# Performance work log

Hardware: AMD Instinct MI355X
Metric: run time of the kernel (lower is better)

The kernel has to match this reference:

```python
import jax, jax.numpy as jnp
import numpy as np

NUM_HEADS = 16


def setup_inputs() -> dict:
    key = jax.random.key(0)
    k1, k2, k3 = jax.random.split(key, 3)
    B, N, C = 2, 2048, 1024
    x = jax.random.normal(k1, (B, N, C), dtype=jnp.float32)
    w_qkv = jax.random.normal(k2, (3 * C, C), dtype=jnp.float32) * (C ** -0.5)
    w_proj = jax.random.normal(k3, (C, C), dtype=jnp.float32) * (C ** -0.5)
    b_proj = jnp.zeros((C,), dtype=jnp.float32)
    return {"x": x, "w_qkv": w_qkv, "w_proj": w_proj, "b_proj": b_proj}


def reference(x, w_qkv, w_proj, b_proj):
    B, N, C = x.shape
    H = NUM_HEADS
    D = C // H
    scale = 1.0 / jnp.sqrt(jnp.asarray(D, x.dtype))
    qkv = (x @ w_qkv.T).reshape(B, N, 3, H, D)
    qkv = jnp.transpose(qkv, (2, 0, 3, 1, 4))  # [3,B,H,N,D]
    q, k, v = qkv[0], qkv[1], qkv[2]
    # scaled dot-product attention with explicit score matrix [B,H,N,N]
    attn = jnp.einsum('bhnd,bhmd->bhnm', q, k) * scale
    attn = jax.nn.softmax(attn, axis=-1)
    out = jnp.einsum('bhnm,bhmd->bhnd', attn, v)
    out = jnp.transpose(out, (0, 2, 1, 3)).reshape(B, N, C)
    # output projection
    return out @ w_proj.T + b_proj
```

## Files before the change

kernel.cpp:

```cpp
#include <hip/hip_runtime.h>

typedef unsigned short u16;
typedef __attribute__((ext_vector_type(8))) short bf16x8;
typedef __attribute__((ext_vector_type(4))) float f32x4;

#define B_ 2
#define N_ 2048
#define C_ 1024
#define H_ 16
#define D_ 64
#define M_ (B_ * N_)

#define QSCALE 0.18033688011114336f

__device__ __forceinline__ u16 f2bf(float f) {
    union { float f; unsigned u; } x; x.f = f;
    return (u16)((x.u + 0x8000u) >> 16);
}
__device__ __forceinline__ unsigned pack2bf(float a, float b) {
    union { float f; unsigned u; } x, y; x.f = a; y.f = b;
    return __builtin_amdgcn_perm(y.u + 0x8000u, x.u + 0x8000u, 0x07060302);
}

__device__ __forceinline__ void async_copy16(const void* gsrc, void* ldst) {
    __builtin_amdgcn_global_load_lds(
        (__attribute__((address_space(1))) void*)gsrc,
        (__attribute__((address_space(3))) void*)ldst,
        16, 0, 0);
}

__global__ void cast3_kernel(const float* __restrict__ x, const float* __restrict__ wq,
                             const float* __restrict__ wp, u16* __restrict__ xo,
                             u16* __restrict__ wqo, u16* __restrict__ wpo) {
    int b = blockIdx.x;
    const float* s; u16* d;
    if (b < 4096)      { s = x;  d = xo;  }
    else if (b < 7168) { s = wq; d = wqo; b -= 4096; }
    else               { s = wp; d = wpo; b -= 7168; }
    int i = (b * 256 + threadIdx.x) * 4;
    const float4 v = *(const float4*)(s + i);
    uint2 o;
    o.x = pack2bf(v.x, v.y);
    o.y = pack2bf(v.z, v.w);
    *(uint2*)(d + i) = o;
}

template <int EPI>
__global__ __launch_bounds__(256, 2) void gemm_bt(
    const u16* __restrict__ A, const u16* __restrict__ Bm,
    int M, int Ncols, int K, int ntiles_n,
    u16* __restrict__ qo, u16* __restrict__ ko, u16* __restrict__ vo,
    const float* __restrict__ bias, float* __restrict__ out) {
    __shared__ u16 As[128 * 64];
    __shared__ u16 Bs[128 * 64];
    const int tid = threadIdx.x, lane = tid & 63, w = tid >> 6;
    const int bx = blockIdx.x % ntiles_n, by = blockIdx.x / ntiles_n;
    const int m0 = by * 128, n0 = bx * 128;
    const int wm = w >> 1, wn = w & 1;
    const int q16 = lane >> 4, l15 = lane & 15;
    const int r0 = lane >> 3, c0 = (lane & 7) * 8;
    f32x4 acc[4][4] = {};

    for (int k0 = 0; k0 < K; k0 += 64) {
#pragma unroll
        for (int i = 0; i < 4; ++i) {
            int blk = w * 4 + i;
            int r = blk * 8 + r0;
            async_copy16(A + (size_t)(m0 + r) * K + k0 + c0, (char*)As + blk * 1024);
            async_copy16(Bm + (size_t)(n0 + r) * K + k0 + c0, (char*)Bs + blk * 1024);
        }
        __builtin_amdgcn_s_waitcnt(0);
        __syncthreads();
#pragma unroll
        for (int ks = 0; ks < 2; ++ks) {
            bf16x8 af[4], bf[4];
#pragma unroll
            for (int i = 0; i < 4; ++i) {
                af[i] = *(const bf16x8*)&As[(wm * 64 + i * 16 + l15) * 64 + ks * 32 + q16 * 8];
                bf[i] = *(const bf16x8*)&Bs[(wn * 64 + i * 16 + l15) * 64 + ks * 32 + q16 * 8];
            }
#pragma unroll
            for (int mi = 0; mi < 4; ++mi)
#pragma unroll
                for (int ni = 0; ni < 4; ++ni)
                    acc[mi][ni] = __builtin_amdgcn_mfma_f32_16x16x32_bf16(af[mi], bf[ni], acc[mi][ni], 0, 0, 0);
        }
        __syncthreads();
    }

#pragma unroll
    for (int mi = 0; mi < 4; ++mi) {
#pragma unroll
        for (int ni = 0; ni < 4; ++ni) {
            int n_g = n0 + wn * 64 + ni * 16 + l15;
#pragma unroll
            for (int r = 0; r < 4; ++r) {
                int m_g = m0 + wm * 64 + mi * 16 + q16 * 4 + r;
                float v = acc[mi][ni][r];
                if (EPI == 0) {
                    int which = n_g >> 10;
                    int h = (n_g >> 6) & 15;
                    int d = n_g & 63;
                    int b = m_g >> 11;
                    int nn = m_g & 2047;
                    size_t idx = ((size_t)((b * H_ + h) * N_ + nn) << 6) + d;
                    if (which == 0)      qo[idx] = f2bf(v * QSCALE);
                    else if (which == 1) ko[idx] = f2bf(v);
                    else                 vo[idx] = f2bf(v);
                } else {
                    out[(size_t)m_g * Ncols + n_g] = v + bias[n_g];
                }
            }
        }
    }
}

__global__ __launch_bounds__(256) void transpose_v(const u16* __restrict__ V, u16* __restrict__ VT) {
    __shared__ u16 tile[64][72];
    const int t = threadIdx.x;
    const int bh = blockIdx.x >> 5;
    const int key0 = (blockIdx.x & 31) * 64;
    const size_t base = (size_t)bh * N_ * D_;
    const int r0 = t >> 3, c8 = (t & 7) * 8;
#pragma unroll
    for (int it = 0; it < 2; ++it) {
        int r = it * 32 + r0;
        uint4 d4 = *(const uint4*)(V + base + (size_t)(key0 + r) * D_ + c8);
        *(uint4*)&tile[r][c8] = d4;
    }
    __syncthreads();
#pragma unroll
    for (int it = 0; it < 2; ++it) {
        int d = it * 32 + r0;
        unsigned t0 = tile[c8 + 0][d], t1 = tile[c8 + 1][d], t2 = tile[c8 + 2][d], t3 = tile[c8 + 3][d];
        unsigned t4 = tile[c8 + 4][d], t5 = tile[c8 + 5][d], t6 = tile[c8 + 6][d], t7 = tile[c8 + 7][d];
        uint4 o;
        o.x = t0 | (t1 << 16); o.y = t2 | (t3 << 16);
        o.z = t4 | (t5 << 16); o.w = t6 | (t7 << 16);
        *(uint4*)(VT + base + (size_t)d * N_ + key0 + c8) = o;
    }
}

__global__ __launch_bounds__(256, 2) void attn_kernel(
    const u16* __restrict__ Q, const u16* __restrict__ K,
    const u16* __restrict__ VT, u16* __restrict__ O) {
    __shared__ u16 Qs[128 * 64];
    __shared__ u16 Ks[128 * 64];
    __shared__ u16 Vs[64 * 128];
    __shared__ u16 Ps[4][32 * 68];
    const int tid = threadIdx.x, lane = tid & 63, w = tid >> 6;
    const int q16 = lane >> 4, l15 = lane & 15;
    const int l7 = l15 & 7;
    const int bh = blockIdx.x >> 4;
    const int q0 = (blockIdx.x & 15) * 128;
    const size_t head = (size_t)bh * N_ * D_;
    const int lr3 = lane >> 3, lc7 = lane & 7;
    const int lr4 = lane >> 4, lc15 = lane & 15;

#pragma unroll
    for (int i = 0; i < 4; ++i) {
        int c = w * 4 + i;
        int row = c * 8 + lr3;
        async_copy16(Q + head + (size_t)(q0 + row) * D_ + (lc7 ^ lr3) * 8, (char*)Qs + c * 1024);
    }
    __builtin_amdgcn_s_waitcnt(0);
    __syncthreads();
    bf16x8 qf[2][2];
#pragma unroll
    for (int f = 0; f < 2; ++f)
#pragma unroll
        for (int ks = 0; ks < 2; ++ks)
            qf[f][ks] = *(const bf16x8*)&Qs[(w * 32 + f * 16 + l15) * 64 + ((ks * 4 + q16) ^ l7) * 8];

    f32x4 o_acc[2][4] = {};
    float rs[2] = {0.f, 0.f};

    for (int kt = 0; kt < 16; ++kt) {
        int key0 = kt * 128;
#pragma unroll
        for (int i = 0; i < 4; ++i) {
            int c = w * 4 + i;
            int krow = c * 8 + lr3;
            async_copy16(K + head + (size_t)(key0 + krow) * D_ + (lc7 ^ lr3) * 8,
                         (char*)Ks + c * 1024);
            int vrow = c * 4 + lr4;
            async_copy16(VT + head + (size_t)vrow * N_ + key0 + (lc15 ^ (vrow & 15)) * 8,
                         (char*)Vs + c * 1024);
        }
        __builtin_amdgcn_s_waitcnt(0);
        __syncthreads();

#pragma unroll
        for (int half = 0; half < 2; ++half) {
#pragma unroll
            for (int kb = 0; kb < 4; ++kb) {
                f32x4 st[2] = {};
#pragma unroll
                for (int ks = 0; ks < 2; ++ks) {
                    bf16x8 kf = *(const bf16x8*)&Ks[((half * 4 + kb) * 16 + l15) * 64 + ((ks * 4 + q16) ^ l7) * 8];
#pragma unroll
                    for (int f = 0; f < 2; ++f)
                        st[f] = __builtin_amdgcn_mfma_f32_16x16x32_bf16(kf, qf[f][ks], st[f], 0, 0, 0);
                }
#pragma unroll
                for (int f = 0; f < 2; ++f) {
                    float p0 = exp2f(st[f][0]), p1 = exp2f(st[f][1]);
                    float p2 = exp2f(st[f][2]), p3 = exp2f(st[f][3]);
                    rs[f] += (p0 + p1) + (p2 + p3);
                    uint2 pk;
                    pk.x = pack2bf(p0, p1);
                    pk.y = pack2bf(p2, p3);
                    *(uint2*)&Ps[w][(f * 16 + l15) * 68 + kb * 16 + q16 * 4] = pk;
                }
            }
#pragma unroll
            for (int ks2 = 0; ks2 < 2; ++ks2) {
                bf16x8 pf[2];
#pragma unroll
                for (int f = 0; f < 2; ++f)
                    pf[f] = *(const bf16x8*)&Ps[w][(f * 16 + l15) * 68 + ks2 * 32 + q16 * 8];
#pragma unroll
                for (int di = 0; di < 4; ++di) {
                    bf16x8 vf = *(const bf16x8*)&Vs[(di * 16 + l15) * 128 + (((half * 2 + ks2) * 4 + q16) ^ l15) * 8];
#pragma unroll
                    for (int f = 0; f < 2; ++f)
                        o_acc[f][di] = __builtin_amdgcn_mfma_f32_16x16x32_bf16(pf[f], vf, o_acc[f][di], 0, 0, 0);
                }
            }
        }
        __syncthreads();
    }

#pragma unroll
    for (int f = 0; f < 2; ++f) {
        rs[f] += __shfl_xor(rs[f], 16);
        rs[f] += __shfl_xor(rs[f], 32);
    }

    const int b = bh >> 4, h = bh & 15;
#pragma unroll
    for (int f = 0; f < 2; ++f) {
        float inv[4];
#pragma unroll
        for (int r = 0; r < 4; ++r) inv[r] = 1.0f / __shfl(rs[f], q16 * 4 + r);
#pragma unroll
        for (int di = 0; di < 4; ++di) {
            int d = di * 16 + l15;
#pragma unroll
            for (int r = 0; r < 4; ++r) {
                int qg = q0 + w * 32 + f * 16 + q16 * 4 + r;
                O[((size_t)(b * N_ + qg) << 10) + h * 64 + d] = f2bf(o_acc[f][di][r] * inv[r]);
            }
        }
    }
}

extern "C" void kernel_launch(void* const* d_in, const int* in_sizes, int n_in,
                              void* d_out, int out_size, void* d_ws, size_t ws_size,
                              hipStream_t stream) {
    const float* x      = (const float*)d_in[0];
    const float* w_qkv  = (const float*)d_in[1];
    const float* w_proj = (const float*)d_in[2];
    const float* b_proj = (const float*)d_in[3];
    float* out = (float*)d_out;

    char* ws = (char*)d_ws;
    const size_t MB = 1024 * 1024;
    u16* x_bf     = (u16*)(ws + 0 * MB);
    u16* wqkv_bf  = (u16*)(ws + 8 * MB);
    u16* wproj_bf = (u16*)(ws + 14 * MB);
    u16* q_bf     = (u16*)(ws + 16 * MB);
    u16* k_bf     = (u16*)(ws + 24 * MB);
    u16* v_bf     = (u16*)(ws + 32 * MB);
    u16* vt_bf    = (u16*)(ws + 40 * MB);
    u16* ao_bf    = (u16*)(ws + 48 * MB);

    cast3_kernel<<<8192, 256, 0, stream>>>(x, w_qkv, w_proj, x_bf, wqkv_bf, wproj_bf);

    gemm_bt<0><<<32 * 24, 256, 0, stream>>>(x_bf, wqkv_bf, M_, 3 * C_, C_, 24,
                                            q_bf, k_bf, v_bf, nullptr, nullptr);

    transpose_v<<<1024, 256, 0, stream>>>(v_bf, vt_bf);

    attn_kernel<<<512, 256, 0, stream>>>(q_bf, k_bf, vt_bf, ao_bf);

    gemm_bt<1><<<32 * 8, 256, 0, stream>>>(ao_bf, wproj_bf, M_, C_, C_, 8,
                                           nullptr, nullptr, nullptr, b_proj, out);
}
```

Measured before the change: 210.3 us.

## Write V transposed from QKV GEMM and double-buffer attention K/V tiles

The QKV GEMM epilogue now writes V directly in transposed [b,h,d,n] layout with packed 8-byte stores, so the separate transpose_v kernel and its extra round trip through memory are dropped. The attention kernel switches to 64-key tiles in double-buffered shared memory, issuing the next tile's async copies before computing on the current one. It also loads Q fragments straight from global memory into registers instead of staging them through shared memory, and raises the occupancy hint to 3 blocks per CU. The trade-off is more loop iterations and barriers per block, plus narrower, more strided V stores in the GEMM epilogue.

```diff
diff --git a/kernel.cpp b/kernel.cpp
--- a/kernel.cpp
+++ b/kernel.cpp
@@ -49,7 +49,7 @@
 __global__ __launch_bounds__(256, 2) void gemm_bt(
     const u16* __restrict__ A, const u16* __restrict__ Bm,
     int M, int Ncols, int K, int ntiles_n,
-    u16* __restrict__ qo, u16* __restrict__ ko, u16* __restrict__ vo,
+    u16* __restrict__ qo, u16* __restrict__ ko, u16* __restrict__ vt,
     const float* __restrict__ bias, float* __restrict__ out) {
     __shared__ u16 As[128 * 64];
     __shared__ u16 Bs[128 * 64];
@@ -93,60 +93,43 @@
 #pragma unroll
         for (int ni = 0; ni < 4; ++ni) {
             int n_g = n0 + wn * 64 + ni * 16 + l15;
-#pragma unroll
-            for (int r = 0; r < 4; ++r) {
-                int m_g = m0 + wm * 64 + mi * 16 + q16 * 4 + r;
-                float v = acc[mi][ni][r];
-                if (EPI == 0) {
-                    int which = n_g >> 10;
-                    int h = (n_g >> 6) & 15;
-                    int d = n_g & 63;
-                    int b = m_g >> 11;
-                    int nn = m_g & 2047;
-                    size_t idx = ((size_t)((b * H_ + h) * N_ + nn) << 6) + d;
-                    if (which == 0)      qo[idx] = f2bf(v * QSCALE);
-                    else if (which == 1) ko[idx] = f2bf(v);
-                    else                 vo[idx] = f2bf(v);
+            if (EPI == 0) {
+                int which = n_g >> 10;
+                int h = (n_g >> 6) & 15;
+                int d = n_g & 63;
+                int m_base = m0 + wm * 64 + mi * 16 + q16 * 4;
+                int b = m_base >> 11;
+                int nn0 = m_base & 2047;
+                if (which == 2) {
+                    uint2 pk;
+                    pk.x = pack2bf(acc[mi][ni][0], acc[mi][ni][1]);
+                    pk.y = pack2bf(acc[mi][ni][2], acc[mi][ni][3]);
+                    *(uint2*)(vt + ((size_t)((b * H_ + h) * D_ + d) << 11) + nn0) = pk;
                 } else {
-                    out[(size_t)m_g * Ncols + n_g] = v + bias[n_g];
+                    size_t base = ((size_t)((b * H_ + h) * N_ + nn0) << 6) + d;
+#pragma unroll
+                    for (int r = 0; r < 4; ++r) {
+                        float v = acc[mi][ni][r];
+                        if (which == 0) qo[base + (size_t)r * D_] = f2bf(v * QSCALE);
+                        else            ko[base + (size_t)r * D_] = f2bf(v);
+                    }
                 }
-            }
-        }
-    }
-}
-
-__global__ __launch_bounds__(256) void transpose_v(const u16* __restrict__ V, u16* __restrict__ VT) {
-    __shared__ u16 tile[64][72];
-    const int t = threadIdx.x;
-    const int bh = blockIdx.x >> 5;
-    const int key0 = (blockIdx.x & 31) * 64;
-    const size_t base = (size_t)bh * N_ * D_;
-    const int r0 = t >> 3, c8 = (t & 7) * 8;
-#pragma unroll
-    for (int it = 0; it < 2; ++it) {
-        int r = it * 32 + r0;
-        uint4 d4 = *(const uint4*)(V + base + (size_t)(key0 + r) * D_ + c8);
-        *(uint4*)&tile[r][c8] = d4;
-    }
-    __syncthreads();
-#pragma unroll
-    for (int it = 0; it < 2; ++it) {
-        int d = it * 32 + r0;
-        unsigned t0 = tile[c8 + 0][d], t1 = tile[c8 + 1][d], t2 = tile[c8 + 2][d], t3 = tile[c8 + 3][d];
-        unsigned t4 = tile[c8 + 4][d], t5 = tile[c8 + 5][d], t6 = tile[c8 + 6][d], t7 = tile[c8 + 7][d];
-        uint4 o;
-        o.x = t0 | (t1 << 16); o.y = t2 | (t3 << 16);
-        o.z = t4 | (t5 << 16); o.w = t6 | (t7 << 16);
-        *(uint4*)(VT + base + (size_t)d * N_ + key0 + c8) = o;
-    }
-}
-
-__global__ __launch_bounds__(256, 2) void attn_kernel(
+            } else {
+#pragma unroll
+                for (int r = 0; r < 4; ++r) {
+                    int m_g = m0 + wm * 64 + mi * 16 + q16 * 4 + r;
+                    out[(size_t)m_g * Ncols + n_g] = acc[mi][ni][r] + bias[n_g];
+                }
+            }
+        }
+    }
+}
+
+__global__ __launch_bounds__(256, 3) void attn_kernel(
     const u16* __restrict__ Q, const u16* __restrict__ K,
     const u16* __restrict__ VT, u16* __restrict__ O) {
-    __shared__ u16 Qs[128 * 64];
-    __shared__ u16 Ks[128 * 64];
-    __shared__ u16 Vs[64 * 128];
+    __shared__ u16 Ks[2][64 * 64];
+    __shared__ u16 Vs[2][64 * 64];
     __shared__ u16 Ps[4][32 * 68];
     const int tid = threadIdx.x, lane = tid & 63, w = tid >> 6;
     const int q16 = lane >> 4, l15 = lane & 15;
@@ -155,79 +138,74 @@
     const int q0 = (blockIdx.x & 15) * 128;
     const size_t head = (size_t)bh * N_ * D_;
     const int lr3 = lane >> 3, lc7 = lane & 7;
-    const int lr4 = lane >> 4, lc15 = lane & 15;
-
-#pragma unroll
-    for (int i = 0; i < 4; ++i) {
-        int c = w * 4 + i;
-        int row = c * 8 + lr3;
-        async_copy16(Q + head + (size_t)(q0 + row) * D_ + (lc7 ^ lr3) * 8, (char*)Qs + c * 1024);
-    }
+
+    auto stage = [&](int kt, int buf) {
+        int key0 = kt * 64;
+#pragma unroll
+        for (int i = 0; i < 2; ++i) {
+            int c = w * 2 + i;
+            int row = c * 8 + lr3;
+            async_copy16(K + head + (size_t)(key0 + row) * D_ + (lc7 ^ lr3) * 8,
+                         (char*)Ks[buf] + c * 1024);
+            async_copy16(VT + head + (size_t)row * N_ + key0 + (lc7 ^ lr3) * 8,
+                         (char*)Vs[buf] + c * 1024);
+        }
+    };
+
+    stage(0, 0);
+    bf16x8 qf[2][2];
+#pragma unroll
+    for (int f = 0; f < 2; ++f)
+#pragma unroll
+        for (int ks = 0; ks < 2; ++ks)
+            qf[f][ks] = *(const bf16x8*)(Q + head + (size_t)(q0 + w * 32 + f * 16 + l15) * D_ +
+                                         ks * 32 + q16 * 8);
     __builtin_amdgcn_s_waitcnt(0);
     __syncthreads();
-    bf16x8 qf[2][2];
-#pragma unroll
-    for (int f = 0; f < 2; ++f)
-#pragma unroll
-        for (int ks = 0; ks < 2; ++ks)
-            qf[f][ks] = *(const bf16x8*)&Qs[(w * 32 + f * 16 + l15) * 64 + ((ks * 4 + q16) ^ l7) * 8];
 
     f32x4 o_acc[2][4] = {};
     float rs[2] = {0.f, 0.f};
 
-    for (int kt = 0; kt < 16; ++kt) {
-        int key0 = kt * 128;
-#pragma unroll
-        for (int i = 0; i < 4; ++i) {
-            int c = w * 4 + i;
-            int krow = c * 8 + lr3;
-            async_copy16(K + head + (size_t)(key0 + krow) * D_ + (lc7 ^ lr3) * 8,
-                         (char*)Ks + c * 1024);
-            int vrow = c * 4 + lr4;
-            async_copy16(VT + head + (size_t)vrow * N_ + key0 + (lc15 ^ (vrow & 15)) * 8,
-                         (char*)Vs + c * 1024);
+    for (int kt = 0; kt < 32; ++kt) {
+        int buf = kt & 1;
+        if (kt + 1 < 32) stage(kt + 1, buf ^ 1);
+
+#pragma unroll
+        for (int kb = 0; kb < 4; ++kb) {
+            f32x4 st[2] = {};
+#pragma unroll
+            for (int ks = 0; ks < 2; ++ks) {
+                bf16x8 kf = *(const bf16x8*)&Ks[buf][(kb * 16 + l15) * 64 + ((ks * 4 + q16) ^ l7) * 8];
+#pragma unroll
+                for (int f = 0; f < 2; ++f)
+                    st[f] = __builtin_amdgcn_mfma_f32_16x16x32_bf16(kf, qf[f][ks], st[f], 0, 0, 0);
+            }
+#pragma unroll
+            for (int f = 0; f < 2; ++f) {
+                float p0 = exp2f(st[f][0]), p1 = exp2f(st[f][1]);
+                float p2 = exp2f(st[f][2]), p3 = exp2f(st[f][3]);
+                rs[f] += (p0 + p1) + (p2 + p3);
+                uint2 pk;
+                pk.x = pack2bf(p0, p1);
+                pk.y = pack2bf(p2, p3);
+                *(uint2*)&Ps[w][(f * 16 + l15) * 68 + kb * 16 + q16 * 4] = pk;
+            }
+        }
+#pragma unroll
+        for (int ks2 = 0; ks2 < 2; ++ks2) {
+            bf16x8 pf[2];
+#pragma unroll
+            for (int f = 0; f < 2; ++f)
+                pf[f] = *(const bf16x8*)&Ps[w][(f * 16 + l15) * 68 + ks2 * 32 + q16 * 8];
+#pragma unroll
+            for (int di = 0; di < 4; ++di) {
+                bf16x8 vf = *(const bf16x8*)&Vs[buf][(di * 16 + l15) * 64 + ((ks2 * 4 + q16) ^ l7) * 8];
+#pragma unroll
+                for (int f = 0; f < 2; ++f)
+                    o_acc[f][di] = __builtin_amdgcn_mfma_f32_16x16x32_bf16(pf[f], vf, o_acc[f][di], 0, 0, 0);
+            }
         }
         __builtin_amdgcn_s_waitcnt(0);
-        __syncthreads();
-
-#pragma unroll
-        for (int half = 0; half < 2; ++half) {
-#pragma unroll
-            for (int kb = 0; kb < 4; ++kb) {
-                f32x4 st[2] = {};
-#pragma unroll
-                for (int ks = 0; ks < 2; ++ks) {
-                    bf16x8 kf = *(const bf16x8*)&Ks[((half * 4 + kb) * 16 + l15) * 64 + ((ks * 4 + q16) ^ l7) * 8];
-#pragma unroll
-                    for (int f = 0; f < 2; ++f)
-                        st[f] = __builtin_amdgcn_mfma_f32_16x16x32_bf16(kf, qf[f][ks], st[f], 0, 0, 0);
-                }
-#pragma unroll
-                for (int f = 0; f < 2; ++f) {
-                    float p0 = exp2f(st[f][0]), p1 = exp2f(st[f][1]);
-                    float p2 = exp2f(st[f][2]), p3 = exp2f(st[f][3]);
-                    rs[f] += (p0 + p1) + (p2 + p3);
-                    uint2 pk;
-                    pk.x = pack2bf(p0, p1);
-                    pk.y = pack2bf(p2, p3);
-                    *(uint2*)&Ps[w][(f * 16 + l15) * 68 + kb * 16 + q16 * 4] = pk;
-                }
-            }
-#pragma unroll
-            for (int ks2 = 0; ks2 < 2; ++ks2) {
-                bf16x8 pf[2];
-#pragma unroll
-                for (int f = 0; f < 2; ++f)
-                    pf[f] = *(const bf16x8*)&Ps[w][(f * 16 + l15) * 68 + ks2 * 32 + q16 * 8];
-#pragma unroll
-                for (int di = 0; di < 4; ++di) {
-                    bf16x8 vf = *(const bf16x8*)&Vs[(di * 16 + l15) * 128 + (((half * 2 + ks2) * 4 + q16) ^ l15) * 8];
-#pragma unroll
-                    for (int f = 0; f < 2; ++f)
-                        o_acc[f][di] = __builtin_amdgcn_mfma_f32_16x16x32_bf16(pf[f], vf, o_acc[f][di], 0, 0, 0);
-                }
-            }
-        }
         __syncthreads();
     }
 
@@ -271,16 +249,13 @@
     u16* wproj_bf = (u16*)(ws + 14 * MB);
     u16* q_bf     = (u16*)(ws + 16 * MB);
     u16* k_bf     = (u16*)(ws + 24 * MB);
-    u16* v_bf     = (u16*)(ws + 32 * MB);
-    u16* vt_bf    = (u16*)(ws + 40 * MB);
-    u16* ao_bf    = (u16*)(ws + 48 * MB);
+    u16* vt_bf    = (u16*)(ws + 32 * MB);
+    u16* ao_bf    = (u16*)(ws + 40 * MB);
 
     cast3_kernel<<<8192, 256, 0, stream>>>(x, w_qkv, w_proj, x_bf, wqkv_bf, wproj_bf);
 
     gemm_bt<0><<<32 * 24, 256, 0, stream>>>(x_bf, wqkv_bf, M_, 3 * C_, C_, 24,
-                                            q_bf, k_bf, v_bf, nullptr, nullptr);
-
-    transpose_v<<<1024, 256, 0, stream>>>(v_bf, vt_bf);
+                                            q_bf, k_bf, vt_bf, nullptr, nullptr);
 
     attn_kernel<<<512, 256, 0, stream>>>(q_bf, k_bf, vt_bf, ao_bf);
 
```

Measured after the change: 211.6 us. About the same (+0.6%).
